# Performance work log

Measured on AMD Instinct MI355X. Metric: run time of the kernel, lower is better.

Reference implementation:

```python
import jax, jax.numpy as jnp
import numpy as np

ISIZE, REC, NACT, BS = 512, 1024, 18, 64
CLIPVAL = 2.0

def setup_inputs() -> dict:
    key = jax.random.key(0)
    ks = jax.random.split(key, 12)
    return {
        "inputs": jax.random.normal(ks[0], (BS, ISIZE), jnp.float32),
        "recurrent_vals": jax.random.normal(ks[1], (BS, REC), jnp.float32),
        "hebb": jax.random.normal(ks[2], (BS, REC, REC), jnp.float32) * 0.1,
        # plastic params
        "w": 0.001 * jax.random.uniform(ks[3], (REC, REC), jnp.float32),
        "alpha": 0.001 * jax.random.uniform(ks[4], (REC, REC), jnp.float32),
        # layer 0: Linear(isize, rec)
        "W0": jax.random.normal(ks[5], (REC, ISIZE), jnp.float32) / np.sqrt(ISIZE),
        "b0": jnp.zeros((REC,), jnp.float32),
        # layer 1: Linear(rec, NBACTIONS)
        "W1": jax.random.normal(ks[6], (NACT, REC), jnp.float32) / np.sqrt(REC),
        "b1": jnp.zeros((NACT,), jnp.float32),
        # h2mod: Linear(rec, 1)
        "h2mod_w": jax.random.normal(ks[7], (1, REC), jnp.float32) / np.sqrt(REC),
        "h2mod_b": jnp.zeros((1,), jnp.float32),
        # modfanout: Linear(1, rec)
        "modfanout_w": jax.random.normal(ks[8], (REC, 1), jnp.float32),
        "modfanout_b": jnp.zeros((REC,), jnp.float32),
    }


def reference(inputs, recurrent_vals, hebb, w, alpha, W0, b0, W1, b1,
              h2mod_w, h2mod_b, modfanout_w, modfanout_b):
    # recurrent layer (i == rec_layer_in == 0):
    # tanh(Linear0(x) + rv @ (w + alpha*hebb))  with per-batch plastic weights
    plastic = w[None, :, :] + alpha[None, :, :] * hebb          # [b, rec, rec]
    rec_in = jnp.einsum('bi,bij->bj', recurrent_vals, plastic)  # [b, rec]
    hactiv = jnp.tanh(inputs @ W0.T + b0 + rec_in)              # [b, rec]
    rec_layer_values = hactiv                                   # i == rec_layer_out
    logits = hactiv @ W1.T + b1                                 # [b, nact]
    act_dis = jax.nn.softmax(logits, axis=1)                    # sf=True
    # neuromodulation
    myeta = jnp.tanh(rec_layer_values @ h2mod_w.T + h2mod_b)    # [b, 1]
    eta = myeta[:, :, None] * modfanout_w.reshape(1, 1, REC) + modfanout_b  # [b,1,rec]
    deltahebb = recurrent_vals[:, :, None] * rec_layer_values[:, None, :]   # [b,rec,rec]
    hebb_return = jnp.clip(hebb + eta * deltahebb, -CLIPVAL, CLIPVAL)
    return act_dis, rec_layer_values, hebb_return
```

## Files before the change

### kernel.cpp

```cpp
#include <hip/hip_runtime.h>
#include <cmath>

constexpr int ISIZE = 512;
constexpr int REC   = 1024;
constexpr int NACT  = 18;
constexpr int BS    = 64;
constexpr float CLIPVAL = 2.0f;
constexpr int NSLOT = 17;
constexpr int GB    = 32;
constexpr int NGR   = BS / GB;

typedef float f4 __attribute__((ext_vector_type(4)));

__device__ __forceinline__ void nt_store(f4* p, f4 v) {
#if __has_builtin(__builtin_nontemporal_store)
  __builtin_nontemporal_store(v, p);
#else
  *p = v;
#endif
}

__global__ __launch_bounds__(256) void k_pass1(
    const float* __restrict__ rv, const float* __restrict__ hebb,
    const float* __restrict__ w, const float* __restrict__ alpha,
    const float* __restrict__ x, const float* __restrict__ W0,
    float* __restrict__ part, int gbase) {
  const int id = blockIdx.x;
  const int t  = threadIdx.x;

  if (id < 256) {
    const int bg = id & 7;
    const int jh = (id >> 3) & 1;
    const int ic = id >> 4;
    const int b0i = gbase + bg * 4, i0 = ic * 64;
    const int jl = t & 127, bl = t >> 7;
    const int j0 = jh * 512 + jl * 4;
    const int ba = b0i + bl * 2;

    __shared__ float rvs[4][64];
    rvs[t >> 6][t & 63] = rv[(size_t)(b0i + (t >> 6)) * REC + i0 + (t & 63)];
    __syncthreads();

    f4 a0 = {0.f, 0.f, 0.f, 0.f}, a1 = {0.f, 0.f, 0.f, 0.f};
    const float* __restrict__ wp  = w     + (size_t)i0 * REC + j0;
    const float* __restrict__ ap  = alpha + (size_t)i0 * REC + j0;
    const float* __restrict__ hp0 = hebb + ((size_t)ba * REC + i0) * REC + j0;
    const float* __restrict__ hp1 = hp0 + (size_t)REC * REC;
    const float* __restrict__ r0s = &rvs[bl * 2][0];
    const float* __restrict__ r1s = &rvs[bl * 2 + 1][0];

#pragma unroll 4
    for (int ii = 0; ii < 64; ++ii) {
      const f4 wv = *(const f4*)(wp  + (size_t)ii * REC);
      const f4 av = *(const f4*)(ap  + (size_t)ii * REC);
      const f4 h0 = *(const f4*)(hp0 + (size_t)ii * REC);
      const f4 h1 = *(const f4*)(hp1 + (size_t)ii * REC);
      const float r0 = r0s[ii], r1 = r1s[ii];
      a0.x = fmaf(r0, fmaf(av.x, h0.x, wv.x), a0.x);
      a0.y = fmaf(r0, fmaf(av.y, h0.y, wv.y), a0.y);
      a0.z = fmaf(r0, fmaf(av.z, h0.z, wv.z), a0.z);
      a0.w = fmaf(r0, fmaf(av.w, h0.w, wv.w), a0.w);
      a1.x = fmaf(r1, fmaf(av.x, h1.x, wv.x), a1.x);
      a1.y = fmaf(r1, fmaf(av.y, h1.y, wv.y), a1.y);
      a1.z = fmaf(r1, fmaf(av.z, h1.z, wv.z), a1.z);
      a1.w = fmaf(r1, fmaf(av.w, h1.w, wv.w), a1.w);
    }
    *(f4*)(part + ((size_t)ba * NSLOT + ic) * REC + j0)       = a0;
    *(f4*)(part + ((size_t)(ba + 1) * NSLOT + ic) * REC + j0) = a1;

  } else {
    const int jt = id - 256;
    const int J0 = jt * 32, B0 = gbase;
    const int tx = t & 31, ty = t >> 5;
    __shared__ float w0s[32][33];
    __shared__ float xs[32][33];
    float acc[4] = {0.f, 0.f, 0.f, 0.f};
    for (int kk = 0; kk < ISIZE; kk += 32) {
#pragma unroll
      for (int r = 0; r < 32; r += 8) {
        w0s[tx][ty + r] = W0[(size_t)(J0 + ty + r) * ISIZE + kk + tx];
        xs[ty + r][tx]  = x [(size_t)(B0 + ty + r) * ISIZE + kk + tx];
      }
      __syncthreads();
#pragma unroll
      for (int k = 0; k < 32; ++k) {
        const float w0v = w0s[k][tx];
#pragma unroll
        for (int q = 0; q < 4; ++q)
          acc[q] = fmaf(xs[ty * 4 + q][k], w0v, acc[q]);
      }
      __syncthreads();
    }
#pragma unroll
    for (int q = 0; q < 4; ++q)
      part[((size_t)(B0 + ty * 4 + q) * NSLOT + 16) * REC + J0 + tx] = acc[q];
  }
}

__global__ __launch_bounds__(1024) void k_head(
    const float* __restrict__ part, const float* __restrict__ b0,
    const float* __restrict__ W1, const float* __restrict__ b1,
    const float* __restrict__ h2w, const float* __restrict__ h2b,
    const float* __restrict__ mw, const float* __restrict__ mb,
    float* __restrict__ hact, float* __restrict__ act_dis,
    float* __restrict__ g, int gbase) {
  const int b = gbase + blockIdx.x;
  const int t = threadIdx.x;
  __shared__ float hsh[REC];
  __shared__ float logits_s[32];
  __shared__ float myeta_s;

  float s = b0[t];
  const float* __restrict__ pb = part + (size_t)b * NSLOT * REC + t;
#pragma unroll
  for (int sl = 0; sl < NSLOT; ++sl) s += pb[(size_t)sl * REC];
  const float h = tanhf(s);
  hact[(size_t)b * REC + t] = h;
  hsh[t] = h;
  __syncthreads();

  const int wv = t >> 6, ln = t & 63;
  for (int a = wv; a < NACT; a += 16) {
    const float* __restrict__ w1a = W1 + (size_t)a * REC;
    float p = 0.f;
#pragma unroll
    for (int c = 0; c < 16; ++c) p = fmaf(hsh[c * 64 + ln], w1a[c * 64 + ln], p);
#pragma unroll
    for (int off = 32; off; off >>= 1) p += __shfl_down(p, off);
    if (ln == 0) logits_s[a] = p + b1[a];
  }
  if (wv == 0) {
    float p = 0.f;
#pragma unroll
    for (int c = 0; c < 16; ++c) p = fmaf(hsh[c * 64 + ln], h2w[c * 64 + ln], p);
#pragma unroll
    for (int off = 32; off; off >>= 1) p += __shfl_down(p, off);
    if (ln == 0) myeta_s = tanhf(p + h2b[0]);
  }
  __syncthreads();

  if (t == 0) {
    float m = logits_s[0];
    for (int a = 1; a < NACT; ++a) m = fmaxf(m, logits_s[a]);
    float e[NACT];
    float ssum = 0.f;
    for (int a = 0; a < NACT; ++a) { e[a] = expf(logits_s[a] - m); ssum += e[a]; }
    const float inv = 1.f / ssum;
    for (int a = 0; a < NACT; ++a) act_dis[(size_t)b * NACT + a] = e[a] * inv;
  }
  __syncthreads();
  const float me = myeta_s;
  g[(size_t)b * REC + t] = fmaf(me, mw[t], mb[t]) * hsh[t];
}

__global__ __launch_bounds__(256) void k_hebb(
    const float* __restrict__ hebb, const float* __restrict__ rv,
    const float* __restrict__ g, float* __restrict__ out, int gbase) {
  const int b  = gbase + blockIdx.x;
  const int i0 = blockIdx.y * 8;
  const int j0 = threadIdx.x * 4;
  const f4 gv = *(const f4*)(g + (size_t)b * REC + j0);
  const float* __restrict__ rvb = rv + (size_t)b * REC;
  const size_t base = ((size_t)b * REC + i0) * REC + j0;
#pragma unroll
  for (int ii = 0; ii < 8; ++ii) {
    const float r = rvb[i0 + ii];
    const f4 hv = *(const f4*)(hebb + base + (size_t)ii * REC);
    f4 o;
    o.x = fminf(fmaxf(fmaf(r, gv.x, hv.x), -CLIPVAL), CLIPVAL);
    o.y = fminf(fmaxf(fmaf(r, gv.y, hv.y), -CLIPVAL), CLIPVAL);
    o.z = fminf(fmaxf(fmaf(r, gv.z, hv.z), -CLIPVAL), CLIPVAL);
    o.w = fminf(fmaxf(fmaf(r, gv.w, hv.w), -CLIPVAL), CLIPVAL);
    nt_store((f4*)(out + base + (size_t)ii * REC), o);
  }
}

extern "C" void kernel_launch(void* const* d_in, const int* in_sizes, int n_in,
                              void* d_out, int out_size, void* d_ws, size_t ws_size,
                              hipStream_t stream) {
  const float* x     = (const float*)d_in[0];
  const float* rv    = (const float*)d_in[1];
  const float* hebb  = (const float*)d_in[2];
  const float* w     = (const float*)d_in[3];
  const float* alpha = (const float*)d_in[4];
  const float* W0    = (const float*)d_in[5];
  const float* b0    = (const float*)d_in[6];
  const float* W1    = (const float*)d_in[7];
  const float* b1    = (const float*)d_in[8];
  const float* h2w   = (const float*)d_in[9];
  const float* h2b   = (const float*)d_in[10];
  const float* mw    = (const float*)d_in[11];
  const float* mb    = (const float*)d_in[12];

  float* out_act  = (float*)d_out;
  float* out_hact = out_act + (size_t)BS * NACT;
  float* out_hebb = out_hact + (size_t)BS * REC;

  float* part = (float*)d_ws;
  float* g    = part + (size_t)BS * NSLOT * REC;

  for (int grp = 0; grp < NGR; ++grp) {
    const int gbase = grp * GB;
    k_pass1<<<288, 256, 0, stream>>>(rv, hebb, w, alpha, x, W0, part, gbase);
    k_head<<<GB, 1024, 0, stream>>>(part, b0, W1, b1, h2w, h2b, mw, mb,
                                    out_hact, out_act, g, gbase);
    k_hebb<<<dim3(GB, 128), 256, 0, stream>>>(hebb, rv, g, out_hebb, gbase);
  }
}
```

Baseline: 164.6 us.

## Fuse stages into one kernel software-pipelined across batch groups of 8

Replaces the three kernels per group of 32 batches with a single multi-role kernel. Each launch runs, on disjoint block ranges, the plastic matvec (pass1) for group k, the head for group k-1 and the hebb update for group k-2. The input-projection GEMM runs once in the first launch. This overlaps the tiny, serial head stage and the launch tails with the bandwidth-heavy hebb streaming, and keeps each group's hebb working set small enough to stay in cache between pass1 and the update. The cost is more launches (10 instead of 6) and fewer blocks per role in each launch, which may leave the GPU under-occupied.

```diff
diff --git a/kernel.cpp b/kernel.cpp
--- a/kernel.cpp
+++ b/kernel.cpp
@@ -7,8 +7,14 @@
 constexpr int BS    = 64;
 constexpr float CLIPVAL = 2.0f;
 constexpr int NSLOT = 17;
-constexpr int GB    = 32;
-constexpr int NGR   = BS / GB;
+constexpr int GB    = 8;
+constexpr int NG    = BS / GB;
+
+constexpr int NB_P2 = 128;
+constexpr int NB_H  = GB;
+constexpr int NB_P1 = 128;
+constexpr int NB_XG = 64;
+constexpr int GRID  = NB_P2 + NB_H + NB_P1 + NB_XG;
 
 typedef float f4 __attribute__((ext_vector_type(4)));
 
@@ -20,57 +26,141 @@
 #endif
 }
 
-__global__ __launch_bounds__(256) void k_pass1(
-    const float* __restrict__ rv, const float* __restrict__ hebb,
-    const float* __restrict__ w, const float* __restrict__ alpha,
-    const float* __restrict__ x, const float* __restrict__ W0,
-    float* __restrict__ part, int gbase) {
+__global__ __launch_bounds__(256) void k_step(
+    const float* __restrict__ x,    const float* __restrict__ rv,
+    const float* __restrict__ hebb, const float* __restrict__ w,
+    const float* __restrict__ alpha,const float* __restrict__ W0,
+    const float* __restrict__ b0,   const float* __restrict__ W1,
+    const float* __restrict__ b1,   const float* __restrict__ h2w,
+    const float* __restrict__ h2b,  const float* __restrict__ mw,
+    const float* __restrict__ mb,   float* __restrict__ part,
+    float* __restrict__ g,          float* __restrict__ hact,
+    float* __restrict__ act_dis,    float* __restrict__ out,
+    int gP1, int gH, int gP2, int doXG) {
   const int id = blockIdx.x;
   const int t  = threadIdx.x;
 
-  if (id < 256) {
-    const int bg = id & 7;
-    const int jh = (id >> 3) & 1;
-    const int ic = id >> 4;
-    const int b0i = gbase + bg * 4, i0 = ic * 64;
-    const int jl = t & 127, bl = t >> 7;
-    const int j0 = jh * 512 + jl * 4;
-    const int ba = b0i + bl * 2;
+  if (id < NB_P2) {
+    if (gP2 < 0) return;
+    const int b  = gP2 * GB + (id & 7);
+    const int i0 = (id >> 3) * 64;
+    const int j0 = t * 4;
+    const f4 gv = *(const f4*)(g + (size_t)b * REC + j0);
+    const float* __restrict__ rvb = rv + (size_t)b * REC + i0;
+    const size_t base = ((size_t)b * REC + i0) * REC + j0;
+#pragma unroll 4
+    for (int ii = 0; ii < 64; ++ii) {
+      const float r = rvb[ii];
+      const f4 hv = *(const f4*)(hebb + base + (size_t)ii * REC);
+      f4 o;
+      o.x = fminf(fmaxf(fmaf(r, gv.x, hv.x), -CLIPVAL), CLIPVAL);
+      o.y = fminf(fmaxf(fmaf(r, gv.y, hv.y), -CLIPVAL), CLIPVAL);
+      o.z = fminf(fmaxf(fmaf(r, gv.z, hv.z), -CLIPVAL), CLIPVAL);
+      o.w = fminf(fmaxf(fmaf(r, gv.w, hv.w), -CLIPVAL), CLIPVAL);
+      nt_store((f4*)(out + base + (size_t)ii * REC), o);
+    }
+
+  } else if (id < NB_P2 + NB_H) {
+    if (gH < 0) return;
+    const int b  = gH * GB + (id - NB_P2);
+    const int j0 = t * 4;
+    __shared__ float hsh[REC];
+    __shared__ float logits_s[32];
+    __shared__ float myeta_s;
+
+    f4 s = *(const f4*)(b0 + j0);
+#pragma unroll
+    for (int sl = 0; sl < NSLOT; ++sl) {
+      const f4 p = *(const f4*)(part + ((size_t)b * NSLOT + sl) * REC + j0);
+      s.x += p.x; s.y += p.y; s.z += p.z; s.w += p.w;
+    }
+    f4 h4;
+    h4.x = tanhf(s.x); h4.y = tanhf(s.y); h4.z = tanhf(s.z); h4.w = tanhf(s.w);
+    *(f4*)(hact + (size_t)b * REC + j0) = h4;
+    *(f4*)(&hsh[j0]) = h4;
+    __syncthreads();
+
+    const int wid = t >> 6, ln = t & 63;
+    for (int a = wid; a < NACT; a += 4) {
+      const float* __restrict__ w1a = W1 + (size_t)a * REC;
+      float p = 0.f;
+#pragma unroll
+      for (int c = 0; c < 16; ++c) p = fmaf(hsh[c * 64 + ln], w1a[c * 64 + ln], p);
+#pragma unroll
+      for (int off = 32; off; off >>= 1) p += __shfl_down(p, off);
+      if (ln == 0) logits_s[a] = p + b1[a];
+    }
+    if (wid == 3) {
+      float p = 0.f;
+#pragma unroll
+      for (int c = 0; c < 16; ++c) p = fmaf(hsh[c * 64 + ln], h2w[c * 64 + ln], p);
+#pragma unroll
+      for (int off = 32; off; off >>= 1) p += __shfl_down(p, off);
+      if (ln == 0) myeta_s = tanhf(p + h2b[0]);
+    }
+    __syncthreads();
+
+    if (t == 0) {
+      float m = logits_s[0];
+      for (int a = 1; a < NACT; ++a) m = fmaxf(m, logits_s[a]);
+      float e[NACT];
+      float ssum = 0.f;
+      for (int a = 0; a < NACT; ++a) { e[a] = expf(logits_s[a] - m); ssum += e[a]; }
+      const float inv = 1.f / ssum;
+      for (int a = 0; a < NACT; ++a) act_dis[(size_t)b * NACT + a] = e[a] * inv;
+    }
+    __syncthreads();
+
+    const float me = myeta_s;
+    const f4 mwv = *(const f4*)(mw + j0);
+    const f4 mbv = *(const f4*)(mb + j0);
+    const f4 hh  = *(const f4*)(&hsh[j0]);
+    f4 gv;
+    gv.x = fmaf(me, mwv.x, mbv.x) * hh.x;
+    gv.y = fmaf(me, mwv.y, mbv.y) * hh.y;
+    gv.z = fmaf(me, mwv.z, mbv.z) * hh.z;
+    gv.w = fmaf(me, mwv.w, mbv.w) * hh.w;
+    *(f4*)(g + (size_t)b * REC + j0) = gv;
+
+  } else if (id < NB_P2 + NB_H + NB_P1) {
+    if (gP1 < 0) return;
+    const int idx = id - (NB_P2 + NB_H);
+    const int bg  = idx & 1;
+    const int jq  = (idx >> 1) & 3;
+    const int ic  = idx >> 3;
+    const int b0i = gP1 * GB + bg * 4;
+    const int i0  = ic * 64;
+    const int jl  = t & 63, blane = t >> 6;
+    const int j0  = jq * 256 + jl * 4;
+    const int ba  = b0i + blane;
 
     __shared__ float rvs[4][64];
     rvs[t >> 6][t & 63] = rv[(size_t)(b0i + (t >> 6)) * REC + i0 + (t & 63)];
     __syncthreads();
 
-    f4 a0 = {0.f, 0.f, 0.f, 0.f}, a1 = {0.f, 0.f, 0.f, 0.f};
-    const float* __restrict__ wp  = w     + (size_t)i0 * REC + j0;
-    const float* __restrict__ ap  = alpha + (size_t)i0 * REC + j0;
-    const float* __restrict__ hp0 = hebb + ((size_t)ba * REC + i0) * REC + j0;
-    const float* __restrict__ hp1 = hp0 + (size_t)REC * REC;
-    const float* __restrict__ r0s = &rvs[bl * 2][0];
-    const float* __restrict__ r1s = &rvs[bl * 2 + 1][0];
-
+    f4 acc = {0.f, 0.f, 0.f, 0.f};
+    const float* __restrict__ wp = w     + (size_t)i0 * REC + j0;
+    const float* __restrict__ ap = alpha + (size_t)i0 * REC + j0;
+    const float* __restrict__ hp = hebb + ((size_t)ba * REC + i0) * REC + j0;
+    const float* __restrict__ rs = &rvs[blane][0];
 #pragma unroll 4
     for (int ii = 0; ii < 64; ++ii) {
-      const f4 wv = *(const f4*)(wp  + (size_t)ii * REC);
-      const f4 av = *(const f4*)(ap  + (size_t)ii * REC);
-      const f4 h0 = *(const f4*)(hp0 + (size_t)ii * REC);
-      const f4 h1 = *(const f4*)(hp1 + (size_t)ii * REC);
-      const float r0 = r0s[ii], r1 = r1s[ii];
-      a0.x = fmaf(r0, fmaf(av.x, h0.x, wv.x), a0.x);
-      a0.y = fmaf(r0, fmaf(av.y, h0.y, wv.y), a0.y);
-      a0.z = fmaf(r0, fmaf(av.z, h0.z, wv.z), a0.z);
-      a0.w = fmaf(r0, fmaf(av.w, h0.w, wv.w), a0.w);
-      a1.x = fmaf(r1, fmaf(av.x, h1.x, wv.x), a1.x);
-      a1.y = fmaf(r1, fmaf(av.y, h1.y, wv.y), a1.y);
-      a1.z = fmaf(r1, fmaf(av.z, h1.z, wv.z), a1.z);
-      a1.w = fmaf(r1, fmaf(av.w, h1.w, wv.w), a1.w);
-    }
-    *(f4*)(part + ((size_t)ba * NSLOT + ic) * REC + j0)       = a0;
-    *(f4*)(part + ((size_t)(ba + 1) * NSLOT + ic) * REC + j0) = a1;
+      const f4 wv = *(const f4*)(wp + (size_t)ii * REC);
+      const f4 av = *(const f4*)(ap + (size_t)ii * REC);
+      const f4 hv = *(const f4*)(hp + (size_t)ii * REC);
+      const float r = rs[ii];
+      acc.x = fmaf(r, fmaf(av.x, hv.x, wv.x), acc.x);
+      acc.y = fmaf(r, fmaf(av.y, hv.y, wv.y), acc.y);
+      acc.z = fmaf(r, fmaf(av.z, hv.z, wv.z), acc.z);
+      acc.w = fmaf(r, fmaf(av.w, hv.w, wv.w), acc.w);
+    }
+    *(f4*)(part + ((size_t)ba * NSLOT + ic) * REC + j0) = acc;
 
   } else {
-    const int jt = id - 256;
-    const int J0 = jt * 32, B0 = gbase;
+    if (!doXG) return;
+    const int idx = id - (NB_P2 + NB_H + NB_P1);
+    const int jt = idx & 31, bh = idx >> 5;
+    const int J0 = jt * 32, B0 = bh * 32;
     const int tx = t & 31, ty = t >> 5;
     __shared__ float w0s[32][33];
     __shared__ float xs[32][33];
@@ -94,84 +184,6 @@
 #pragma unroll
     for (int q = 0; q < 4; ++q)
       part[((size_t)(B0 + ty * 4 + q) * NSLOT + 16) * REC + J0 + tx] = acc[q];
-  }
-}
-
-__global__ __launch_bounds__(1024) void k_head(
-    const float* __restrict__ part, const float* __restrict__ b0,
-    const float* __restrict__ W1, const float* __restrict__ b1,
-    const float* __restrict__ h2w, const float* __restrict__ h2b,
-    const float* __restrict__ mw, const float* __restrict__ mb,
-    float* __restrict__ hact, float* __restrict__ act_dis,
-    float* __restrict__ g, int gbase) {
-  const int b = gbase + blockIdx.x;
-  const int t = threadIdx.x;
-  __shared__ float hsh[REC];
-  __shared__ float logits_s[32];
-  __shared__ float myeta_s;
-
-  float s = b0[t];
-  const float* __restrict__ pb = part + (size_t)b * NSLOT * REC + t;
-#pragma unroll
-  for (int sl = 0; sl < NSLOT; ++sl) s += pb[(size_t)sl * REC];
-  const float h = tanhf(s);
-  hact[(size_t)b * REC + t] = h;
-  hsh[t] = h;
-  __syncthreads();
-
-  const int wv = t >> 6, ln = t & 63;
-  for (int a = wv; a < NACT; a += 16) {
-    const float* __restrict__ w1a = W1 + (size_t)a * REC;
-    float p = 0.f;
-#pragma unroll
-    for (int c = 0; c < 16; ++c) p = fmaf(hsh[c * 64 + ln], w1a[c * 64 + ln], p);
-#pragma unroll
-    for (int off = 32; off; off >>= 1) p += __shfl_down(p, off);
-    if (ln == 0) logits_s[a] = p + b1[a];
-  }
-  if (wv == 0) {
-    float p = 0.f;
-#pragma unroll
-    for (int c = 0; c < 16; ++c) p = fmaf(hsh[c * 64 + ln], h2w[c * 64 + ln], p);
-#pragma unroll
-    for (int off = 32; off; off >>= 1) p += __shfl_down(p, off);
-    if (ln == 0) myeta_s = tanhf(p + h2b[0]);
-  }
-  __syncthreads();
-
-  if (t == 0) {
-    float m = logits_s[0];
-    for (int a = 1; a < NACT; ++a) m = fmaxf(m, logits_s[a]);
-    float e[NACT];
-    float ssum = 0.f;
-    for (int a = 0; a < NACT; ++a) { e[a] = expf(logits_s[a] - m); ssum += e[a]; }
-    const float inv = 1.f / ssum;
-    for (int a = 0; a < NACT; ++a) act_dis[(size_t)b * NACT + a] = e[a] * inv;
-  }
-  __syncthreads();
-  const float me = myeta_s;
-  g[(size_t)b * REC + t] = fmaf(me, mw[t], mb[t]) * hsh[t];
-}
-
-__global__ __launch_bounds__(256) void k_hebb(
-    const float* __restrict__ hebb, const float* __restrict__ rv,
-    const float* __restrict__ g, float* __restrict__ out, int gbase) {
-  const int b  = gbase + blockIdx.x;
-  const int i0 = blockIdx.y * 8;
-  const int j0 = threadIdx.x * 4;
-  const f4 gv = *(const f4*)(g + (size_t)b * REC + j0);
-  const float* __restrict__ rvb = rv + (size_t)b * REC;
-  const size_t base = ((size_t)b * REC + i0) * REC + j0;
-#pragma unroll
-  for (int ii = 0; ii < 8; ++ii) {
-    const float r = rvb[i0 + ii];
-    const f4 hv = *(const f4*)(hebb + base + (size_t)ii * REC);
-    f4 o;
-    o.x = fminf(fmaxf(fmaf(r, gv.x, hv.x), -CLIPVAL), CLIPVAL);
-    o.y = fminf(fmaxf(fmaf(r, gv.y, hv.y), -CLIPVAL), CLIPVAL);
-    o.z = fminf(fmaxf(fmaf(r, gv.z, hv.z), -CLIPVAL), CLIPVAL);
-    o.w = fminf(fmaxf(fmaf(r, gv.w, hv.w), -CLIPVAL), CLIPVAL);
-    nt_store((f4*)(out + base + (size_t)ii * REC), o);
   }
 }
 
@@ -199,11 +211,14 @@
   float* part = (float*)d_ws;
   float* g    = part + (size_t)BS * NSLOT * REC;
 
-  for (int grp = 0; grp < NGR; ++grp) {
-    const int gbase = grp * GB;
-    k_pass1<<<288, 256, 0, stream>>>(rv, hebb, w, alpha, x, W0, part, gbase);
-    k_head<<<GB, 1024, 0, stream>>>(part, b0, W1, b1, h2w, h2b, mw, mb,
-                                    out_hact, out_act, g, gbase);
-    k_hebb<<<dim3(GB, 128), 256, 0, stream>>>(hebb, rv, g, out_hebb, gbase);
+  for (int k = 0; k < NG + 2; ++k) {
+    const int gP1 = (k < NG) ? k : -1;
+    const int gH  = (k >= 1 && k <= NG) ? k - 1 : -1;
+    const int gP2 = (k >= 2) ? k - 2 : -1;
+    const int doXG = (k == 0) ? 1 : 0;
+    k_step<<<GRID, 256, 0, stream>>>(x, rv, hebb, w, alpha, W0, b0, W1, b1,
+                                     h2w, h2b, mw, mb, part, g,
+                                     out_hact, out_act, out_hebb,
+                                     gP1, gH, gP2, doXG);
   }
 }
```

Measured after the change: 216.0 us. +31.2%, slower.
